# Optimization experiments

Hardware: AMD Instinct MI355X
Metric: run time of the kernel (lower is better)

Reference implementation:

```python
import jax, jax.numpy as jnp
import numpy as np

B, C, Ci, H, W = 8, 256, 128, 64, 64
EPS = 1e-5


def conv1x1(x, w, b):
    # x: [B,C,H,W], w: [O,C], b: [O] -> [B,O,H,W]
    return jnp.einsum('bchw,oc->bohw', x, w) + b[None, :, None, None]


def maxpool2(x):
    b, c, h, w = x.shape
    return x.reshape(b, c, h // 2, 2, w // 2, 2).max(axis=(3, 5))


def setup_inputs() -> dict:
    key = jax.random.key(0)
    ks = jax.random.split(key, 12)
    s_in = 1.0 / np.sqrt(C)
    s_ic = 1.0 / np.sqrt(Ci)
    return {
        'x': jax.random.normal(ks[0], (B, C, H, W), dtype=jnp.float32),
        'g_w': jax.random.normal(ks[1], (Ci, C), dtype=jnp.float32) * s_in,
        'g_b': jax.random.normal(ks[2], (Ci,), dtype=jnp.float32) * 0.01,
        'theta_w': jax.random.normal(ks[3], (Ci, C), dtype=jnp.float32) * s_in,
        'theta_b': jax.random.normal(ks[4], (Ci,), dtype=jnp.float32) * 0.01,
        'phi_w': jax.random.normal(ks[5], (Ci, C), dtype=jnp.float32) * s_in,
        'phi_b': jax.random.normal(ks[6], (Ci,), dtype=jnp.float32) * 0.01,
        'W_w': jax.random.normal(ks[7], (C, Ci), dtype=jnp.float32) * s_ic,
        'W_b': jax.random.normal(ks[8], (C,), dtype=jnp.float32) * 0.01,
        'bn_gamma': jax.random.normal(ks[9], (C,), dtype=jnp.float32) * 0.1 + 1.0,
        'bn_beta': jax.random.normal(ks[10], (C,), dtype=jnp.float32) * 0.1,
        'bn_mean': jnp.zeros((C,), dtype=jnp.float32),
        'bn_var': jax.random.uniform(ks[11], (C,), dtype=jnp.float32) * 0.5 + 0.75,
    }


def reference(x, g_w, g_b, theta_w, theta_b, phi_w, phi_b, W_w, W_b, bn_gamma, bn_beta, bn_mean, bn_var):
    b = x.shape[0]
    # g and phi: 1x1 conv then 2x2 max-pool (sub_sample=True)
    g_x = maxpool2(conv1x1(x, g_w, g_b)).reshape(b, Ci, -1)          # [B,Ci,Np]
    g_x = jnp.transpose(g_x, (0, 2, 1))                               # [B,Np,Ci]
    theta_x = conv1x1(x, theta_w, theta_b).reshape(b, Ci, -1)         # [B,Ci,N]
    theta_x = jnp.transpose(theta_x, (0, 2, 1))                       # [B,N,Ci]
    phi_x = maxpool2(conv1x1(x, phi_w, phi_b)).reshape(b, Ci, -1)     # [B,Ci,Np]
    f = jnp.einsum('bnc,bcm->bnm', theta_x, phi_x)                    # [B,N,Np]
    f_div_C = jax.nn.softmax(f, axis=-1)                              # embedded_gaussian: plain softmax, no scaling
    y = jnp.einsum('bnm,bmc->bnc', f_div_C, g_x)                      # [B,N,Ci]
    y = jnp.transpose(y, (0, 2, 1)).reshape(b, Ci, H, W)              # [B,Ci,H,W]
    # W: 1x1 conv + BatchNorm (inference form with running stats)
    W_y = conv1x1(y, W_w, W_b)
    inv = bn_gamma / jnp.sqrt(bn_var + EPS)
    W_y = (W_y - bn_mean[None, :, None, None]) * inv[None, :, None, None] + bn_beta[None, :, None, None]
    return W_y + x
```

## Files before the change

kernel.cpp:

```cpp
#include <hip/hip_runtime.h>
#include <math.h>

#define Bn   8
#define Cc   256
#define Cin  128
#define Hh   64
#define Ww   64
#define Nn   4096
#define Npl  1024
#define EPSf 1e-5f

typedef __attribute__((ext_vector_type(8))) short    short8;
typedef __attribute__((ext_vector_type(8))) _Float16 half8;
typedef __attribute__((ext_vector_type(4))) float    floatx4;

__device__ __forceinline__ unsigned short f2bf(float f) {
    unsigned int u = __float_as_uint(f);
    u += 0x7fffu + ((u >> 16) & 1u);
    return (unsigned short)(u >> 16);
}
__device__ __forceinline__ unsigned short f2h(float f) {
    _Float16 h = (_Float16)f;
    return __builtin_bit_cast(unsigned short, h);
}
__device__ __forceinline__ float h2f(unsigned short u) {
    return (float)__builtin_bit_cast(_Float16, u);
}

__global__ __launch_bounds__(256) void k_prep(
    const float* __restrict__ g_w, const float* __restrict__ th_w,
    const float* __restrict__ ph_w,
    const float* __restrict__ W_w, const float* __restrict__ W_b,
    const float* __restrict__ gamma, const float* __restrict__ beta,
    const float* __restrict__ mean,  const float* __restrict__ var,
    unsigned short* __restrict__ gWh,
    unsigned short* __restrict__ thWh, unsigned short* __restrict__ thWl,
    unsigned short* __restrict__ phWh, unsigned short* __restrict__ phWl,
    unsigned short* __restrict__ Wh, float* __restrict__ cvec)
{
    int i = blockIdx.x * 256 + threadIdx.x;
    if (i < 98304) {
        int seg = i >> 15;
        int idx = i & 32767;
        float v = (seg == 0 ? g_w : (seg == 1 ? th_w : ph_w))[idx];
        unsigned short hi = f2h(v);
        if (seg == 0) gWh[idx] = hi;
        else {
            (seg == 1 ? thWh : phWh)[idx] = hi;
            (seg == 1 ? thWl : phWl)[idx] = f2h(v - h2f(hi));
        }
    } else {
        int j = i - 98304;
        int o = j >> 7;
        float inv = gamma[o] * rsqrtf(var[o] + EPSf);
        Wh[j] = f2h(W_w[j] * inv);
        if (j < Cc) {
            float invi = gamma[j] * rsqrtf(var[j] + EPSf);
            cvec[j] = (W_b[j] - mean[j]) * invi + beta[j];
        }
    }
}

#define XPAD 264

__global__ __launch_bounds__(256, 2) void k_conv3(
    const float* __restrict__ x,
    const unsigned short* __restrict__ gWh,
    const unsigned short* __restrict__ thWh, const unsigned short* __restrict__ thWl,
    const unsigned short* __restrict__ phWh, const unsigned short* __restrict__ phWl,
    const float* __restrict__ g_b, const float* __restrict__ th_b,
    const float* __restrict__ ph_b,
    unsigned short* __restrict__ thetaT,
    unsigned short* __restrict__ gPc,
    unsigned short* __restrict__ phiPt)
{
    __shared__ __align__(16) unsigned short Xhi[64 * XPAD];
    __shared__ __align__(16) unsigned short Xlo[64 * XPAD];

    const int t    = threadIdx.x;
    const int w    = t >> 6;
    const int l    = t & 63;
    const int quad = l >> 4;
    const int l16  = l & 15;
    const int b    = blockIdx.x >> 6;
    const int tile = blockIdx.x & 63;
    const int ty   = tile >> 1;
    const int tx   = tile & 1;

    {
        const float4* xg = (const float4*)x;
        unsigned int* XhiW = (unsigned int*)Xhi;
        unsigned int* XloW = (unsigned int*)Xlo;
        #pragma unroll
        for (int it = 0; it < 8; ++it) {
            int idx = t + 256 * it;
            int c2  = idx >> 4;
            int p4  = idx & 15;
            int n   = (2 * ty + (p4 >> 3)) * Ww + tx * 32 + (p4 & 7) * 4;
            float4 va = xg[((size_t)(b * Cc + 2 * c2) * Nn + n) >> 2];
            float4 vb = xg[((size_t)(b * Cc + 2 * c2 + 1) * Nn + n) >> 2];
            const float fa[4] = {va.x, va.y, va.z, va.w};
            const float fb[4] = {vb.x, vb.y, vb.z, vb.w};
            #pragma unroll
            for (int i = 0; i < 4; ++i) {
                int px = p4 * 4 + i;
                unsigned short ha = f2h(fa[i]), hb = f2h(fb[i]);
                unsigned short la = f2h(fa[i] - h2f(ha));
                unsigned short lb = f2h(fb[i] - h2f(hb));
                XhiW[px * 132 + c2] = (unsigned int)ha | ((unsigned int)hb << 16);
                XloW[px * 132 + c2] = (unsigned int)la | ((unsigned int)lb << 16);
            }
        }
    }
    __syncthreads();

    floatx4 acc[6][4] = {};

    #pragma unroll 2
    for (int kd = 0; kd < 8; ++kd) {
        half8 bhi[4], blo[4];
        #pragma unroll
        for (int nt = 0; nt < 4; ++nt) {
            bhi[nt] = *(const half8*)&Xhi[(nt * 16 + l16) * XPAD + kd * 32 + quad * 8];
            blo[nt] = *(const half8*)&Xlo[(nt * 16 + l16) * XPAD + kd * 32 + quad * 8];
        }
        #pragma unroll
        for (int ti = 0; ti < 6; ++ti) {
            int ot  = w + 4 * ti;
            int seg = ot >> 3;
            size_t aoff = (size_t)((ot & 7) * 16 + l16) * Cc + kd * 32 + quad * 8;
            const unsigned short* wh = (seg == 0 ? gWh : (seg == 1 ? thWh : phWh));
            half8 ah = *(const half8*)&wh[aoff];
            #pragma unroll
            for (int nt = 0; nt < 4; ++nt)
                acc[ti][nt] = __builtin_amdgcn_mfma_f32_16x16x32_f16(ah, bhi[nt], acc[ti][nt], 0, 0, 0);
            if (seg != 0) {
                const unsigned short* wl = (seg == 1 ? thWl : phWl);
                half8 al = *(const half8*)&wl[aoff];
                #pragma unroll
                for (int nt = 0; nt < 4; ++nt) {
                    acc[ti][nt] = __builtin_amdgcn_mfma_f32_16x16x32_f16(ah, blo[nt], acc[ti][nt], 0, 0, 0);
                    acc[ti][nt] = __builtin_amdgcn_mfma_f32_16x16x32_f16(al, bhi[nt], acc[ti][nt], 0, 0, 0);
                }
            }
        }
    }

    #pragma unroll
    for (int ti = 0; ti < 6; ++ti) {
        int ot  = w + 4 * ti;
        int seg = ot >> 3;
        int ol  = (ot & 7) * 16 + quad * 4;
        if (seg == 1) {
            float b0 = th_b[ol], b1 = th_b[ol + 1], b2 = th_b[ol + 2], b3 = th_b[ol + 3];
            #pragma unroll
            for (int nt = 0; nt < 4; ++nt) {
                int n = (2 * ty + (nt >> 1)) * Ww + tx * 32 + (nt & 1) * 16 + l16;
                ushort4 v;
                v.x = f2h(acc[ti][nt][0] + b0);
                v.y = f2h(acc[ti][nt][1] + b1);
                v.z = f2h(acc[ti][nt][2] + b2);
                v.w = f2h(acc[ti][nt][3] + b3);
                *(ushort4*)&thetaT[((size_t)b * Nn + n) * Cin + ol] = v;
            }
        } else {
            const float* bb = (seg == 0 ? g_b : ph_b);
            float b0 = bb[ol], b1 = bb[ol + 1], b2 = bb[ol + 2], b3 = bb[ol + 3];
            #pragma unroll
            for (int pp = 0; pp < 2; ++pp) {
                float pm[4];
                #pragma unroll
                for (int r = 0; r < 4; ++r) {
                    float m = fmaxf(acc[ti][pp][r], acc[ti][pp + 2][r]);
                    pm[r] = fmaxf(m, __shfl_xor(m, 1, 64));
                }
                int np = ty * 32 + tx * 16 + pp * 8 + (l16 >> 1);
                if ((l16 & 1) == 0) {
                    if (seg == 0) {
                        gPc[((size_t)b * Cin + ol + 0) * Npl + np] = f2bf(pm[0] + b0);
                        gPc[((size_t)b * Cin + ol + 1) * Npl + np] = f2bf(pm[1] + b1);
                        gPc[((size_t)b * Cin + ol + 2) * Npl + np] = f2bf(pm[2] + b2);
                        gPc[((size_t)b * Cin + ol + 3) * Npl + np] = f2bf(pm[3] + b3);
                    } else {
                        ushort4 v;
                        v.x = f2h(pm[0] + b0); v.y = f2h(pm[1] + b1);
                        v.z = f2h(pm[2] + b2); v.w = f2h(pm[3] + b3);
                        *(ushort4*)&phiPt[((size_t)b * Npl + np) * Cin + ol] = v;
                    }
                }
            }
        }
    }
}

#define DPAD 136
#define VPAD 72
#define PPAD 68
#define SSHIFT 20.0f

__global__ __launch_bounds__(256, 3) void k_attn(
    const unsigned short* __restrict__ thetaT,
    const unsigned short* __restrict__ phiPt,
    const unsigned short* __restrict__ gPc,
    unsigned short* __restrict__ Yh, float* __restrict__ Lpart)
{
    __shared__ __align__(16) unsigned short Ks[64 * DPAD];
    __shared__ __align__(16) unsigned short Vt[Cin * VPAD];
    __shared__ __align__(16) unsigned short Ps[4][16 * PPAD];

    const int t    = threadIdx.x;
    const int w    = t >> 6;
    const int l    = t & 63;
    const int quad = l >> 4;
    const int l16  = l & 15;
    const int b    = blockIdx.x >> 7;
    const int kh   = (blockIdx.x >> 6) & 1;
    const int qb   = blockIdx.x & 63;
    const int n0   = qb * 64;

    uint4 qr[4];
    #pragma unroll
    for (int kd = 0; kd < 4; ++kd)
        qr[kd] = *(const uint4*)&thetaT[((size_t)b * Nn + n0 + w * 16 + l16) * Cin
                                        + kd * 32 + quad * 8];
    #pragma unroll
    for (int kd = 0; kd < 4; ++kd)
        asm volatile("" : "+v"(qr[kd].x), "+v"(qr[kd].y), "+v"(qr[kd].z), "+v"(qr[kd].w));
    half8 qf[4];
    #pragma unroll
    for (int kd = 0; kd < 4; ++kd) qf[kd] = __builtin_bit_cast(half8, qr[kd]);

    floatx4 yacc[8] = {};
    float li[4] = {0.f, 0.f, 0.f, 0.f};

    for (int ch = 0; ch < 8; ++ch) {
        const int chg = kh * 8 + ch;
        __syncthreads();
        #pragma unroll
        for (int it = 0; it < 4; ++it) {
            int idx = t + 256 * it;
            int m = idx >> 4, d8 = idx & 15;
            *(uint4*)&Ks[m * DPAD + d8 * 8] =
                *(const uint4*)&phiPt[((size_t)b * Npl + chg * 64 + m) * Cin + d8 * 8];
        }
        #pragma unroll
        for (int it = 0; it < 4; ++it) {
            int idx = t + 256 * it;
            int c = idx >> 3, m8 = idx & 7;
            *(uint4*)&Vt[c * VPAD + m8 * 8] =
                *(const uint4*)&gPc[((size_t)b * Cin + c) * Npl + chg * 64 + m8 * 8];
        }
        __syncthreads();

        floatx4 sacc[4] = {};
        #pragma unroll
        for (int mt = 0; mt < 4; ++mt) {
            #pragma unroll
            for (int kd = 0; kd < 4; ++kd) {
                half8 kf = *(const half8*)&Ks[(mt * 16 + l16) * DPAD + kd * 32 + quad * 8];
                sacc[mt] = __builtin_amdgcn_mfma_f32_16x16x32_f16(qf[kd], kf, sacc[mt], 0, 0, 0);
            }
        }

        #pragma unroll
        for (int mt = 0; mt < 4; ++mt) {
            #pragma unroll
            for (int r = 0; r < 4; ++r) {
                float e = __expf(sacc[mt][r] - SSHIFT);
                li[r] += e;
                Ps[w][(quad * 4 + r) * PPAD + mt * 16 + l16] = f2bf(e);
            }
        }

        short8 pf[2];
        #pragma unroll
        for (int kd = 0; kd < 2; ++kd)
            pf[kd] = *(const short8*)&Ps[w][l16 * PPAD + kd * 32 + quad * 8];

        #pragma unroll
        for (int ct = 0; ct < 8; ++ct) {
            #pragma unroll
            for (int kd = 0; kd < 2; ++kd) {
                short8 vf = *(const short8*)&Vt[(ct * 16 + l16) * VPAD + kd * 32 + quad * 8];
                yacc[ct] = __builtin_amdgcn_mfma_f32_16x16x32_bf16(pf[kd], vf, yacc[ct], 0, 0, 0);
            }
        }
    }

    unsigned short* Yp = Yh + ((size_t)(kh * Bn + b) * Nn) * Cin;
    float* Lp = Lpart + (size_t)(kh * Bn + b) * Nn;
    #pragma unroll
    for (int r = 0; r < 4; ++r) {
        #pragma unroll
        for (int o = 1; o < 16; o <<= 1) li[r] += __shfl_xor(li[r], o, 64);
        float il = 1.0f / li[r];
        int q = n0 + w * 16 + quad * 4 + r;
        #pragma unroll
        for (int ct = 0; ct < 8; ++ct)
            Yp[(size_t)q * Cin + ct * 16 + l16] = f2h(yacc[ct][r] * il);
        if (l16 == 0) Lp[q] = li[r];
    }
}

__global__ __launch_bounds__(256) void k_out(
    const unsigned short* __restrict__ Yh, const float* __restrict__ Lpart,
    const float* __restrict__ x,
    const unsigned short* __restrict__ Wh, const float* __restrict__ cvec,
    float* __restrict__ out)
{
    __shared__ __align__(16) unsigned short Ys[64 * DPAD];
    __shared__ __align__(16) unsigned short Ws[128 * DPAD];
    __shared__ float w0s[64], w1s[64];

    const int t    = threadIdx.x;
    const int w    = t >> 6;
    const int l    = t & 63;
    const int quad = l >> 4;
    const int l16  = l & 15;
    const int b    = blockIdx.x >> 6;
    const int qt   = blockIdx.x & 63;
    const int n0   = qt * 64;

    if (t < 64) {
        float l0 = Lpart[(size_t)b * Nn + n0 + t];
        float l1 = Lpart[(size_t)(Bn + b) * Nn + n0 + t];
        float s  = 1.0f / (l0 + l1);
        w0s[t] = l0 * s;
        w1s[t] = l1 * s;
    }
    __syncthreads();

    {
        const uint4* Y0 = (const uint4*)(Yh + ((size_t)b * Nn) * Cin);
        const uint4* Y1 = (const uint4*)(Yh + ((size_t)(Bn + b) * Nn) * Cin);
        #pragma unroll
        for (int it = 0; it < 4; ++it) {
            int idx = t + 256 * it;
            int q  = idx >> 4;
            int d8 = idx & 15;
            size_t gi = (((size_t)(n0 + q) * Cin) >> 3) + d8;
            half8 a = __builtin_bit_cast(half8, Y0[gi]);
            half8 c = __builtin_bit_cast(half8, Y1[gi]);
            float w0 = w0s[q], w1 = w1s[q];
            half8 r;
            #pragma unroll
            for (int i = 0; i < 8; ++i)
                r[i] = (_Float16)(w0 * (float)a[i] + w1 * (float)c[i]);
            *(uint4*)&Ys[q * DPAD + d8 * 8] = __builtin_bit_cast(uint4, r);
        }
    }

    for (int oc = 0; oc < 2; ++oc) {
        __syncthreads();
        #pragma unroll
        for (int it = 0; it < 8; ++it) {
            int idx = t + 256 * it;
            int o = idx >> 4, d8 = idx & 15;
            *(uint4*)&Ws[o * DPAD + d8 * 8] =
                *(const uint4*)&Wh[((size_t)(oc * 128 + o)) * Cin + d8 * 8];
        }
        __syncthreads();

        half8 af[2][4];
        #pragma unroll
        for (int mt = 0; mt < 2; ++mt)
            #pragma unroll
            for (int kd = 0; kd < 4; ++kd)
                af[mt][kd] = *(const half8*)&Ws[(w * 32 + mt * 16 + l16) * DPAD + kd * 32 + quad * 8];

        floatx4 acc[2][4] = {};
        #pragma unroll
        for (int nt = 0; nt < 4; ++nt) {
            half8 bfr[4];
            #pragma unroll
            for (int kd = 0; kd < 4; ++kd)
                bfr[kd] = *(const half8*)&Ys[(nt * 16 + l16) * DPAD + kd * 32 + quad * 8];
            #pragma unroll
            for (int mt = 0; mt < 2; ++mt)
                #pragma unroll
                for (int kd = 0; kd < 4; ++kd)
                    acc[mt][nt] = __builtin_amdgcn_mfma_f32_16x16x32_f16(af[mt][kd], bfr[kd], acc[mt][nt], 0, 0, 0);
        }

        #pragma unroll
        for (int mt = 0; mt < 2; ++mt) {
            #pragma unroll
            for (int r = 0; r < 4; ++r) {
                int o = oc * 128 + w * 32 + mt * 16 + quad * 4 + r;
                float cv = cvec[o];
                #pragma unroll
                for (int nt = 0; nt < 4; ++nt) {
                    size_t gi = ((size_t)(b * Cc + o)) * Nn + n0 + nt * 16 + l16;
                    out[gi] = acc[mt][nt][r] + cv + x[gi];
                }
            }
        }
    }
}

extern "C" void kernel_launch(void* const* d_in, const int* in_sizes, int n_in,
                              void* d_out, int out_size, void* d_ws, size_t ws_size,
                              hipStream_t stream) {
    const float* x    = (const float*)d_in[0];
    const float* g_w  = (const float*)d_in[1];
    const float* g_b  = (const float*)d_in[2];
    const float* th_w = (const float*)d_in[3];
    const float* th_b = (const float*)d_in[4];
    const float* ph_w = (const float*)d_in[5];
    const float* ph_b = (const float*)d_in[6];
    const float* W_w  = (const float*)d_in[7];
    const float* W_b  = (const float*)d_in[8];
    const float* gmm  = (const float*)d_in[9];
    const float* bta  = (const float*)d_in[10];
    const float* mmn  = (const float*)d_in[11];
    const float* vvr  = (const float*)d_in[12];
    float* out = (float*)d_out;

    unsigned short* thetaT = (unsigned short*)d_ws;
    unsigned short* phiPt  = thetaT + (size_t)4194304;
    unsigned short* gPc    = phiPt + (size_t)1048576;
    unsigned short* Wh     = gPc + (size_t)1048576;
    unsigned short* gWh    = Wh + 32768;
    unsigned short* thWh   = gWh + 32768;
    unsigned short* thWl   = thWh + 32768;
    unsigned short* phWh   = thWl + 32768;
    unsigned short* phWl   = phWh + 32768;
    float*          cvec   = (float*)(phWl + 32768);
    unsigned short* Yh     = (unsigned short*)(cvec + 256);
    float*          Lpart  = (float*)(Yh + (size_t)2 * Bn * Nn * Cin);

    k_prep<<<dim3(512), dim3(256), 0, stream>>>(
        g_w, th_w, ph_w, W_w, W_b, gmm, bta, mmn, vvr,
        gWh, thWh, thWl, phWh, phWl, Wh, cvec);
    k_conv3<<<dim3(Bn * 64), dim3(256), 0, stream>>>(
        x, gWh, thWh, thWl, phWh, phWl, g_b, th_b, ph_b, thetaT, gPc, phiPt);
    k_attn<<<dim3(Bn * 128), dim3(256), 0, stream>>>(thetaT, phiPt, gPc, Yh, Lpart);
    k_out<<<dim3(Bn * 64), dim3(256), 0, stream>>>(Yh, Lpart, x, Wh, cvec, out);
}
```

Measured before the change: 180.8 us.

## Use direct global-to-LDS loads with XOR swizzle and register-only softmax probabilities

K and V tiles are now loaded with global_load_lds straight into unpadded, XOR-swizzled shared memory instead of staging through registers. The QK MFMA operands are swapped so each lane holds scores for one query, and the probabilities are packed to bf16 and rearranged with permlane swaps instead of a round trip through shared memory. Row sums shrink to one accumulator per lane, and the smaller LDS footprint allows raising the occupancy hint to 4 blocks per SIMD. The price is more complex lane shuffles and a full vmcnt wait before each barrier, with no overlap of the loads.

```diff
diff --git a/kernel.cpp b/kernel.cpp
--- a/kernel.cpp
+++ b/kernel.cpp
@@ -25,6 +25,18 @@
 }
 __device__ __forceinline__ float h2f(unsigned short u) {
     return (float)__builtin_bit_cast(_Float16, u);
+}
+
+__device__ __forceinline__ unsigned int cvtpk_bf16(float lo, float hi) {
+    unsigned int r;
+    asm("v_cvt_pk_bf16_f32 %0, %1, %2" : "=v"(r) : "v"(lo), "v"(hi));
+    return r;
+}
+
+__device__ __forceinline__ void gload_lds16(const unsigned short* g, unsigned short* l) {
+    __builtin_amdgcn_global_load_lds(
+        (const __attribute__((address_space(1))) unsigned int*)g,
+        (__attribute__((address_space(3))) unsigned int*)l, 16, 0, 0);
 }
 
 __global__ __launch_bounds__(256) void k_prep(
@@ -193,20 +205,16 @@
     }
 }
 
-#define DPAD 136
-#define VPAD 72
-#define PPAD 68
 #define SSHIFT 20.0f
 
-__global__ __launch_bounds__(256, 3) void k_attn(
+__global__ __launch_bounds__(256, 4) void k_attn(
     const unsigned short* __restrict__ thetaT,
     const unsigned short* __restrict__ phiPt,
     const unsigned short* __restrict__ gPc,
     unsigned short* __restrict__ Yh, float* __restrict__ Lpart)
 {
-    __shared__ __align__(16) unsigned short Ks[64 * DPAD];
-    __shared__ __align__(16) unsigned short Vt[Cin * VPAD];
-    __shared__ __align__(16) unsigned short Ps[4][16 * PPAD];
+    __shared__ __align__(16) unsigned short Ks[64 * 128];
+    __shared__ __align__(16) unsigned short Vt[128 * 64];
 
     const int t    = threadIdx.x;
     const int w    = t >> 6;
@@ -231,25 +239,29 @@
     for (int kd = 0; kd < 4; ++kd) qf[kd] = __builtin_bit_cast(half8, qr[kd]);
 
     floatx4 yacc[8] = {};
-    float li[4] = {0.f, 0.f, 0.f, 0.f};
+    float liq = 0.f;
 
     for (int ch = 0; ch < 8; ++ch) {
         const int chg = kh * 8 + ch;
         __syncthreads();
-        #pragma unroll
-        for (int it = 0; it < 4; ++it) {
-            int idx = t + 256 * it;
-            int m = idx >> 4, d8 = idx & 15;
-            *(uint4*)&Ks[m * DPAD + d8 * 8] =
-                *(const uint4*)&phiPt[((size_t)b * Npl + chg * 64 + m) * Cin + d8 * 8];
-        }
-        #pragma unroll
-        for (int it = 0; it < 4; ++it) {
-            int idx = t + 256 * it;
-            int c = idx >> 3, m8 = idx & 7;
-            *(uint4*)&Vt[c * VPAD + m8 * 8] =
-                *(const uint4*)&gPc[((size_t)b * Cin + c) * Npl + chg * 64 + m8 * 8];
-        }
+
+        #pragma unroll
+        for (int j = 0; j < 4; ++j) {
+            int slot = w * 4 + j;
+            int m  = slot * 4 + (l >> 4);
+            int gs = (l & 15) ^ (m & 7);
+            gload_lds16(&phiPt[((size_t)b * Npl + chg * 64 + m) * Cin + gs * 8],
+                        &Ks[slot * 512]);
+        }
+        #pragma unroll
+        for (int j = 0; j < 4; ++j) {
+            int slot = w * 4 + j;
+            int c  = slot * 8 + (l >> 3);
+            int gs = (l & 7) ^ (c & 7);
+            gload_lds16(&gPc[((size_t)b * Cin + c) * Npl + chg * 64 + gs * 8],
+                        &Vt[slot * 512]);
+        }
+        asm volatile("s_waitcnt vmcnt(0)" ::: "memory");
         __syncthreads();
 
         floatx4 sacc[4] = {};
@@ -257,50 +269,67 @@
         for (int mt = 0; mt < 4; ++mt) {
             #pragma unroll
             for (int kd = 0; kd < 4; ++kd) {
-                half8 kf = *(const half8*)&Ks[(mt * 16 + l16) * DPAD + kd * 32 + quad * 8];
-                sacc[mt] = __builtin_amdgcn_mfma_f32_16x16x32_f16(qf[kd], kf, sacc[mt], 0, 0, 0);
-            }
-        }
-
+                half8 kf = *(const half8*)&Ks[(mt * 16 + l16) * 128
+                                              + ((kd * 4 + quad) ^ (l16 & 7)) * 8];
+                sacc[mt] = __builtin_amdgcn_mfma_f32_16x16x32_f16(kf, qf[kd], sacc[mt], 0, 0, 0);
+            }
+        }
+
+        float ex[4][4];
         #pragma unroll
         for (int mt = 0; mt < 4; ++mt) {
             #pragma unroll
             for (int r = 0; r < 4; ++r) {
-                float e = __expf(sacc[mt][r] - SSHIFT);
-                li[r] += e;
-                Ps[w][(quad * 4 + r) * PPAD + mt * 16 + l16] = f2bf(e);
+                float v = __expf(sacc[mt][r] - SSHIFT);
+                ex[mt][r] = v;
+                liq += v;
             }
         }
 
         short8 pf[2];
         #pragma unroll
-        for (int kd = 0; kd < 2; ++kd)
-            pf[kd] = *(const short8*)&Ps[w][l16 * PPAD + kd * 32 + quad * 8];
+        for (int kd = 0; kd < 2; ++kd) {
+            unsigned int a0 = cvtpk_bf16(ex[2 * kd][0],     ex[2 * kd][1]);
+            unsigned int a1 = cvtpk_bf16(ex[2 * kd + 1][0], ex[2 * kd + 1][1]);
+            unsigned int b0 = cvtpk_bf16(ex[2 * kd][2],     ex[2 * kd][3]);
+            unsigned int b1 = cvtpk_bf16(ex[2 * kd + 1][2], ex[2 * kd + 1][3]);
+            asm volatile("v_permlane32_swap_b32 %0, %1" : "+v"(a0), "+v"(a1));
+            asm volatile("v_permlane16_swap_b32 %0, %1" : "+v"(a0), "+v"(a1));
+            asm volatile("v_permlane32_swap_b32 %0, %1" : "+v"(b0), "+v"(b1));
+            asm volatile("v_permlane16_swap_b32 %0, %1" : "+v"(b0), "+v"(b1));
+            uint4 pw; pw.x = a0; pw.y = b0; pw.z = a1; pw.w = b1;
+            pf[kd] = __builtin_bit_cast(short8, pw);
+        }
 
         #pragma unroll
         for (int ct = 0; ct < 8; ++ct) {
             #pragma unroll
             for (int kd = 0; kd < 2; ++kd) {
-                short8 vf = *(const short8*)&Vt[(ct * 16 + l16) * VPAD + kd * 32 + quad * 8];
+                short8 vf = *(const short8*)&Vt[(ct * 16 + l16) * 64
+                                                + ((kd * 4 + quad) ^ (l16 & 7)) * 8];
                 yacc[ct] = __builtin_amdgcn_mfma_f32_16x16x32_bf16(pf[kd], vf, yacc[ct], 0, 0, 0);
             }
         }
     }
+
+    liq += __shfl_xor(liq, 16, 64);
+    liq += __shfl_xor(liq, 32, 64);
 
     unsigned short* Yp = Yh + ((size_t)(kh * Bn + b) * Nn) * Cin;
     float* Lp = Lpart + (size_t)(kh * Bn + b) * Nn;
     #pragma unroll
     for (int r = 0; r < 4; ++r) {
-        #pragma unroll
-        for (int o = 1; o < 16; o <<= 1) li[r] += __shfl_xor(li[r], o, 64);
-        float il = 1.0f / li[r];
+        float lr = __shfl(liq, quad * 4 + r, 64);
+        float il = 1.0f / lr;
         int q = n0 + w * 16 + quad * 4 + r;
         #pragma unroll
         for (int ct = 0; ct < 8; ++ct)
             Yp[(size_t)q * Cin + ct * 16 + l16] = f2h(yacc[ct][r] * il);
-        if (l16 == 0) Lp[q] = li[r];
-    }
-}
+        if (l16 == 0) Lp[q] = lr;
+    }
+}
+
+#define DPAD 136
 
 __global__ __launch_bounds__(256) void k_out(
     const unsigned short* __restrict__ Yh, const float* __restrict__ Lpart,
```

New measurement: 168.7 us. 1.07x faster.
